# Kernel optimization log

Hardware: AMD Instinct MI355X
Metric: run time of the kernel (lower is better)

Reference implementation:

```python
import jax, jax.numpy as jnp
import numpy as np
import itertools, functools, operator

NUM_RBF = 32
CUTOFF = 5.0
METRIC = (1, 1, 1)


def _count_bits(x):
    return bin(x).count("1")


def _sign_euclidean(a, b):
    a >>= 1
    s = 0
    while a:
        s += _count_bits(a & b)
        a >>= 1
    return 1 if (s & 1) == 0 else -1


def build_cayley(metric):
    """Dense [2^n, 2^n, 2^n] geometric multiplication (Cayley) table, shortlex blade order."""
    n = len(metric)
    blade_sets = itertools.chain.from_iterable(
        itertools.combinations([1 << i for i in range(n)], r) for r in range(n + 1)
    )
    index_to_bitmap = [functools.reduce(operator.or_, t, 0) for t in blade_sets]
    bitmap_to_index = {b: i for i, b in enumerate(index_to_bitmap)}
    N = 2 ** n
    cayley = np.zeros((N, N, N), dtype=np.float32)
    for i in range(N):
        bi = index_to_bitmap[i]
        for j in range(N):
            bj = index_to_bitmap[j]
            sign = _sign_euclidean(bi, bj)
            bm = bi & bj
            k = 0
            while bm:
                if bm & 1:
                    sign *= metric[k]
                k += 1
                bm >>= 1
            cayley[i, bitmap_to_index[bi ^ bj], j] = sign
    return cayley


CAYLEY = jnp.asarray(build_cayley(METRIC))  # [8,8,8], sparse +/-1 structure


def geometric_product(a, b):
    # torch: einsum('...i,ijk,...k->...j', a, cayley, b)
    return jnp.einsum('...i,ijk,...k->...j', a, CAYLEY, b)


def setup_inputs() -> dict:
    key = jax.random.key(0)
    k0, k1, k2, k3, k4, k5 = jax.random.split(key, 6)
    N, E, C = 50000, 800000, 16
    h = jax.random.normal(k0, (N, C, 8), jnp.float32)
    pos = jax.random.uniform(k1, (N, 3), jnp.float32) * 10.0
    edge_index = jax.random.randint(k2, (2, E), 0, N, jnp.int32)
    W_rbf = jax.random.normal(k3, (NUM_RBF, C), jnp.float32) / np.sqrt(NUM_RBF)
    W_out = jax.random.normal(k4, (C, C), jnp.float32) / np.sqrt(C)
    W_sgp = jax.random.normal(k5, (C, C), jnp.float32) / np.sqrt(C)
    return {"h": h, "pos": pos, "edge_index": edge_index,
            "W_rbf": W_rbf, "W_out": W_out, "W_sgp": W_sgp}


def reference(h, pos, edge_index, W_rbf, W_out, W_sgp):
    N, C, B = h.shape
    src, dst = edge_index[0], edge_index[1]

    # relative geometry
    rel = pos[dst] - pos[src]                                  # [E,3]
    dist = jnp.sqrt(jnp.sum(rel * rel, axis=-1) + 1e-12)       # [E]

    # embed unit relative vector as a grade-1 multivector (blades 1..3)
    rel_mv = jnp.zeros((rel.shape[0], 1, B), h.dtype)
    rel_mv = rel_mv.at[:, 0, 1:4].set(rel / dist[:, None])     # [E,1,8]

    # radial weights: gaussian smearing -> linear -> cosine cutoff envelope
    mus = jnp.linspace(0.0, CUTOFF, NUM_RBF, dtype=h.dtype)
    gamma = (NUM_RBF / CUTOFF) ** 2
    rbf = jnp.exp(-gamma * (dist[:, None] - mus) ** 2)         # [E,32]
    env = 0.5 * (jnp.cos(jnp.pi * dist / CUTOFF) + 1.0) * (dist < CUTOFF)
    w_e = (rbf @ W_rbf) * env[:, None]                          # [E,C]

    # equivariant messages: geometric product against edge multivector
    msg = geometric_product(h[src], rel_mv) * w_e[..., None]   # [E,C,8]
    agg = jax.ops.segment_sum(msg, dst, num_segments=N)        # [N,C,8]

    # MVLinear channel mixing (shared across blades)
    out = jnp.einsum('nci,co->noi', agg, W_out)                # [N,C,8]

    # MACE-style higher-order: steerable geometric product self-interaction
    q = jnp.einsum('nci,co->noi', h, W_sgp)                    # [N,C,8]
    return out + geometric_product(out, q)
```

## Files before the change

kernel.cpp:

```cpp
#include <hip/hip_runtime.h>

#define CUTOFF 5.0f
#define GAMMA 40.96f
#define MU_STEP 0.16129032f
#define INV_MU 6.2f
#define PI_F 3.14159265358979f
#define MAXDEG 24


__global__ __launch_bounds__(256) void k_fill_geom(
    const float* __restrict__ pos, const int* __restrict__ ei,
    int* __restrict__ deg, int* __restrict__ rec,
    float4* __restrict__ edata, int E)
{
    int e = blockIdx.x * 256 + threadIdx.x;
    if (e >= E) return;
    int src = ei[e], dst = ei[E + e];
    float dx = pos[dst*3+0] - pos[src*3+0];
    float dy = pos[dst*3+1] - pos[src*3+1];
    float dz = pos[dst*3+2] - pos[src*3+2];
    float d = sqrtf(dx*dx + dy*dy + dz*dz + 1e-12f);
    if (d < CUTOFF) {
        int slot = atomicAdd(&deg[dst], 1);
        if (slot < MAXDEG) {
            const float s = (0.5f * (__cosf(PI_F * d * (1.0f/CUTOFF)) + 1.0f)) / d;
            rec[dst*MAXDEG + slot] = src;
            edata[(size_t)dst*MAXDEG + slot] = make_float4(dx*s, dy*s, dz*s, d);
        }
    }
}

__global__ __launch_bounds__(256) void k_gather_finalize(
    const float* __restrict__ h,
    const int* __restrict__ rec, const int* __restrict__ deg,
    const float4* __restrict__ edata,
    const float* __restrict__ Wrbf, const float* __restrict__ Wout,
    const float* __restrict__ Wsgp, float* __restrict__ out, int N)
{
    __shared__ float s_wr[512];
    __shared__ float s_Wout[256];
    __shared__ float s_Wsgp[256];
    __shared__ float s_agg[16*132];
    __shared__ float s_h[16*132];

    const int t  = threadIdx.x;
    const int nl = t >> 4;
    const int c  = t & 15;
    const int lane  = t & 63;
    const int gbase = lane & 48;
    const long long nodeBase = (long long)blockIdx.x * 16;
    const long long n = nodeBase + nl;

    s_wr[t]       = Wrbf[t];
    s_wr[t + 256] = Wrbf[t + 256];
    s_Wout[t] = Wout[t];
    s_Wsgp[t] = Wsgp[t];

    for (int idx = t; idx < 512; idx += 256) {
        int nn = idx >> 5;
        int r  = idx & 31;
        long long node = nodeBase + nn;
        float4 vh = make_float4(0,0,0,0);
        if (node < N) vh = *(const float4*)(h + node*128 + (long long)r*4);
        *(float4*)(&s_h[nn*132 + r*4]) = vh;
    }
    __syncthreads();

    float m0=0,m1=0,m2=0,m3=0,m4=0,m5=0,m6=0,m7=0;
    if (n < N) {
        const int start = (int)n * MAXDEG;
        const int dg    = min(deg[n], MAXDEG);
        const int dgE   = dg & ~1;

        for (int base = 0; base < dgE; base += 2) {
            const int2 ss  = *(const int2*)(rec + start + base);
            const float4 g0 = edata[start + base];
            const float4 g1 = edata[start + base + 1];

            const float4* hp0 = (const float4*)(h + (((long long)ss.x*16 + c) << 3));
            const float4* hp1 = (const float4*)(h + (((long long)ss.y*16 + c) << 3));
            const float4 A0 = hp0[0], B0 = hp0[1];
            const float4 A1 = hp1[0], B1 = hp1[1];

            const int kl0 = min(max(0, __float2int_rn(g0.w * INV_MU) - 2), 27);
            const int kl1 = min(max(0, __float2int_rn(g1.w * INV_MU) - 2), 27);

            const int   sel   = c >> 3;
            const float dsel  = sel ? g1.w : g0.w;
            const int   klsel = sel ? kl1 : kl0;
            const float xx = dsel - MU_STEP * (float)(klsel + (c & 7));
            const float ee = __expf(-GAMMA * xx * xx);

            float w0 = 0.0f, w1 = 0.0f;
            #pragma unroll
            for (int j = 0; j < 5; ++j) {
                const float e0 = __shfl(ee, gbase + j);
                const float e1 = __shfl(ee, gbase + 8 + j);
                w0 += e0 * s_wr[(kl0 + j)*16 + c];
                w1 += e1 * s_wr[(kl1 + j)*16 + c];
            }

            m0 += (A0.y*g0.x + A0.z*g0.y + A0.w*g0.z)*w0 + (A1.y*g1.x + A1.z*g1.y + A1.w*g1.z)*w1;
            m1 += (A0.x*g0.x + B0.x*g0.y + B0.y*g0.z)*w0 + (A1.x*g1.x + B1.x*g1.y + B1.y*g1.z)*w1;
            m2 += (A0.x*g0.y - B0.x*g0.x + B0.z*g0.z)*w0 + (A1.x*g1.y - B1.x*g1.x + B1.z*g1.z)*w1;
            m3 += (A0.x*g0.z - B0.y*g0.x - B0.z*g0.y)*w0 + (A1.x*g1.z - B1.y*g1.x - B1.z*g1.y)*w1;
            m4 += (A0.y*g0.y - A0.z*g0.x + B0.w*g0.z)*w0 + (A1.y*g1.y - A1.z*g1.x + B1.w*g1.z)*w1;
            m5 += (A0.y*g0.z - A0.w*g0.x - B0.w*g0.y)*w0 + (A1.y*g1.z - A1.w*g1.x - B1.w*g1.y)*w1;
            m6 += (A0.z*g0.z - A0.w*g0.y + B0.w*g0.x)*w0 + (A1.z*g1.z - A1.w*g1.y + B1.w*g1.x)*w1;
            m7 += (B0.z*g0.x - B0.y*g0.y + B0.x*g0.z)*w0 + (B1.z*g1.x - B1.y*g1.y + B1.x*g1.z)*w1;
        }

        if (dg & 1) {
            const int s0 = rec[start + dgE];
            const float4 g0 = edata[start + dgE];
            const float4* hp0 = (const float4*)(h + (((long long)s0*16 + c) << 3));
            const float4 A0 = hp0[0], B0 = hp0[1];

            const int kl0 = min(max(0, __float2int_rn(g0.w * INV_MU) - 2), 27);
            const float xx = g0.w - MU_STEP * (float)(kl0 + (c & 7));
            const float ee = __expf(-GAMMA * xx * xx);

            float w0 = 0.0f;
            #pragma unroll
            for (int j = 0; j < 5; ++j)
                w0 += __shfl(ee, gbase + j) * s_wr[(kl0 + j)*16 + c];

            m0 += (A0.y*g0.x + A0.z*g0.y + A0.w*g0.z)*w0;
            m1 += (A0.x*g0.x + B0.x*g0.y + B0.y*g0.z)*w0;
            m2 += (A0.x*g0.y - B0.x*g0.x + B0.z*g0.z)*w0;
            m3 += (A0.x*g0.z - B0.y*g0.x - B0.z*g0.y)*w0;
            m4 += (A0.y*g0.y - A0.z*g0.x + B0.w*g0.z)*w0;
            m5 += (A0.y*g0.z - A0.w*g0.x - B0.w*g0.y)*w0;
            m6 += (A0.z*g0.z - A0.w*g0.y + B0.w*g0.x)*w0;
            m7 += (B0.z*g0.x - B0.y*g0.y + B0.x*g0.z)*w0;
        }
    }

    __syncthreads();
    float* ag = &s_agg[nl*132 + c*8];
    *(float4*)(ag)     = make_float4(m0, m1, m2, m3);
    *(float4*)(ag + 4) = make_float4(m4, m5, m6, m7);
    __syncthreads();

    const int o = c;
    const float* A = &s_agg[nl*132];
    const float* H = &s_h[nl*132];

    float o0=0,o1=0,o2=0,o3=0,o4=0,o5=0,o6=0,o7=0;
    float q0=0,q1=0,q2=0,q3=0,q4=0,q5=0,q6=0,q7=0;
    #pragma unroll
    for (int cc = 0; cc < 16; ++cc) {
        const float wo = s_Wout[cc*16 + o];
        const float ws = s_Wsgp[cc*16 + o];
        const float* a  = A + cc*8;
        const float* hh = H + cc*8;
        o0 += a[0]*wo; o1 += a[1]*wo; o2 += a[2]*wo; o3 += a[3]*wo;
        o4 += a[4]*wo; o5 += a[5]*wo; o6 += a[6]*wo; o7 += a[7]*wo;
        q0 += hh[0]*ws; q1 += hh[1]*ws; q2 += hh[2]*ws; q3 += hh[3]*ws;
        q4 += hh[4]*ws; q5 += hh[5]*ws; q6 += hh[6]*ws; q7 += hh[7]*ws;
    }

    const float r0 = o0 + (o0*q0 + o1*q1 + o2*q2 + o3*q3 - o4*q4 - o5*q5 - o6*q6 - o7*q7);
    const float r1 = o1 + (o0*q1 + o1*q0 - o2*q4 - o3*q5 + o4*q2 + o5*q3 - o6*q7 - o7*q6);
    const float r2 = o2 + (o0*q2 + o1*q4 + o2*q0 - o3*q6 - o4*q1 + o5*q7 + o6*q3 + o7*q5);
    const float r3 = o3 + (o0*q3 + o1*q5 + o2*q6 + o3*q0 - o4*q7 - o5*q1 - o6*q2 - o7*q4);
    const float r4 = o4 + (o0*q4 + o1*q2 - o2*q1 + o3*q7 + o4*q0 - o5*q6 + o6*q5 + o7*q3);
    const float r5 = o5 + (o0*q5 + o1*q3 - o2*q7 - o3*q1 + o4*q6 + o5*q0 - o6*q4 - o7*q2);
    const float r6 = o6 + (o0*q6 + o1*q7 + o2*q3 - o3*q2 - o4*q5 + o5*q4 + o6*q0 + o7*q1);
    const float r7 = o7 + (o0*q7 + o1*q6 - o2*q5 + o3*q4 + o4*q3 - o5*q2 + o6*q1 + o7*q0);

    if (n < N) {
        float* op = out + (n*16 + o)*8;
        *(float4*)(op)     = make_float4(r0, r1, r2, r3);
        *(float4*)(op + 4) = make_float4(r4, r5, r6, r7);
    }
}

extern "C" void kernel_launch(void* const* d_in, const int* in_sizes, int n_in,
                              void* d_out, int out_size, void* d_ws, size_t ws_size,
                              hipStream_t stream) {
    const float* h    = (const float*)d_in[0];
    const float* pos  = (const float*)d_in[1];
    const int*   ei   = (const int*)d_in[2];
    const float* Wrbf = (const float*)d_in[3];
    const float* Wout = (const float*)d_in[4];
    const float* Wsgp = (const float*)d_in[5];
    float* out = (float*)d_out;

    const int N = in_sizes[0] / 128;
    const int E = in_sizes[2] / 2;

    float4* edata = (float4*)d_ws;
    int* deg = (int*)(edata + (size_t)N * MAXDEG);
    int* rec = deg + N;

    hipMemsetAsync(deg, 0, (size_t)N * sizeof(int), stream);

    const int eBlocks = (E + 255) / 256;
    k_fill_geom<<<eBlocks, 256, 0, stream>>>(pos, ei, deg, rec, edata, E);

    const int gBlocks = (N + 15) / 16;
    k_gather_finalize<<<gBlocks, 256, 0, stream>>>(
        h, rec, deg, edata, Wrbf, Wout, Wsgp, out, N);
}
```

Baseline: 138.1 us.

## Split fused gather/finalize kernel into separate edge-gather and finalize kernels

The fused gather+finalize kernel is split in two. The edge gather writes per-node aggregates into the output buffer, and a second kernel reloads them together with h to do the channel mixing and the self-interaction geometric product. The aim is to cut shared memory and register pressure in the gather kernel so it can run with higher occupancy. The cost is an extra kernel launch and an extra round trip of the aggregate through global memory.

```diff
diff --git a/kernel.cpp b/kernel.cpp
--- a/kernel.cpp
+++ b/kernel.cpp
@@ -30,40 +30,24 @@
     }
 }
 
-__global__ __launch_bounds__(256) void k_gather_finalize(
+__global__ __launch_bounds__(256) void k_edge_gather(
     const float* __restrict__ h,
     const int* __restrict__ rec, const int* __restrict__ deg,
     const float4* __restrict__ edata,
-    const float* __restrict__ Wrbf, const float* __restrict__ Wout,
-    const float* __restrict__ Wsgp, float* __restrict__ out, int N)
+    const float* __restrict__ Wrbf,
+    float* __restrict__ out, int N)
 {
     __shared__ float s_wr[512];
-    __shared__ float s_Wout[256];
-    __shared__ float s_Wsgp[256];
-    __shared__ float s_agg[16*132];
-    __shared__ float s_h[16*132];
 
     const int t  = threadIdx.x;
     const int nl = t >> 4;
     const int c  = t & 15;
     const int lane  = t & 63;
     const int gbase = lane & 48;
-    const long long nodeBase = (long long)blockIdx.x * 16;
-    const long long n = nodeBase + nl;
+    const long long n = (long long)blockIdx.x * 16 + nl;
 
     s_wr[t]       = Wrbf[t];
     s_wr[t + 256] = Wrbf[t + 256];
-    s_Wout[t] = Wout[t];
-    s_Wsgp[t] = Wsgp[t];
-
-    for (int idx = t; idx < 512; idx += 256) {
-        int nn = idx >> 5;
-        int r  = idx & 31;
-        long long node = nodeBase + nn;
-        float4 vh = make_float4(0,0,0,0);
-        if (node < N) vh = *(const float4*)(h + node*128 + (long long)r*4);
-        *(float4*)(&s_h[nn*132 + r*4]) = vh;
-    }
     __syncthreads();
 
     float m0=0,m1=0,m2=0,m3=0,m4=0,m5=0,m6=0,m7=0;
@@ -134,24 +118,57 @@
             m6 += (A0.z*g0.z - A0.w*g0.y + B0.w*g0.x)*w0;
             m7 += (B0.z*g0.x - B0.y*g0.y + B0.x*g0.z)*w0;
         }
-    }
-
+
+        float* op = out + n*128 + (long long)c*8;
+        *(float4*)(op)     = make_float4(m0, m1, m2, m3);
+        *(float4*)(op + 4) = make_float4(m4, m5, m6, m7);
+    }
+}
+
+__global__ __launch_bounds__(256) void k_finalize(
+    const float* __restrict__ h,
+    const float* __restrict__ Wout, const float* __restrict__ Wsgp,
+    float* __restrict__ out, int N)
+{
+    __shared__ float s_Wout[256];
+    __shared__ float s_Wsgp[256];
+    __shared__ float s_a[16*132];
+    __shared__ float s_h[16*132];
+
+    const int t  = threadIdx.x;
+    const int nl = t >> 4;
+    const int c  = t & 15;
+    const long long nodeBase = (long long)blockIdx.x * 16;
+    const long long n = nodeBase + nl;
+
+    s_Wout[t] = Wout[t];
+    s_Wsgp[t] = Wsgp[t];
+
+    for (int idx = t; idx < 1024; idx += 256) {
+        const int half = idx >> 9;
+        const int j    = idx & 511;
+        const int nn   = j >> 5;
+        const int r    = j & 31;
+        const long long node = nodeBase + nn;
+        float4 v = make_float4(0,0,0,0);
+        if (node < N) {
+            const float* src = half ? (h + node*128) : (out + node*128);
+            v = *(const float4*)(src + (long long)r*4);
+        }
+        float* dst = half ? &s_h[nn*132 + r*4] : &s_a[nn*132 + r*4];
+        *(float4*)(dst) = v;
+    }
     __syncthreads();
-    float* ag = &s_agg[nl*132 + c*8];
-    *(float4*)(ag)     = make_float4(m0, m1, m2, m3);
-    *(float4*)(ag + 4) = make_float4(m4, m5, m6, m7);
-    __syncthreads();
-
-    const int o = c;
-    const float* A = &s_agg[nl*132];
+
+    const float* A = &s_a[nl*132];
     const float* H = &s_h[nl*132];
 
     float o0=0,o1=0,o2=0,o3=0,o4=0,o5=0,o6=0,o7=0;
     float q0=0,q1=0,q2=0,q3=0,q4=0,q5=0,q6=0,q7=0;
     #pragma unroll
     for (int cc = 0; cc < 16; ++cc) {
-        const float wo = s_Wout[cc*16 + o];
-        const float ws = s_Wsgp[cc*16 + o];
+        const float wo = s_Wout[cc*16 + c];
+        const float ws = s_Wsgp[cc*16 + c];
         const float* a  = A + cc*8;
         const float* hh = H + cc*8;
         o0 += a[0]*wo; o1 += a[1]*wo; o2 += a[2]*wo; o3 += a[3]*wo;
@@ -170,7 +187,7 @@
     const float r7 = o7 + (o0*q7 + o1*q6 - o2*q5 + o3*q4 + o4*q3 - o5*q2 + o6*q1 + o7*q0);
 
     if (n < N) {
-        float* op = out + (n*16 + o)*8;
+        float* op = out + (n*16 + c)*8;
         *(float4*)(op)     = make_float4(r0, r1, r2, r3);
         *(float4*)(op + 4) = make_float4(r4, r5, r6, r7);
     }
@@ -200,6 +217,8 @@
     k_fill_geom<<<eBlocks, 256, 0, stream>>>(pos, ei, deg, rec, edata, E);
 
     const int gBlocks = (N + 15) / 16;
-    k_gather_finalize<<<gBlocks, 256, 0, stream>>>(
-        h, rec, deg, edata, Wrbf, Wout, Wsgp, out, N);
-}
+    k_edge_gather<<<gBlocks, 256, 0, stream>>>(
+        h, rec, deg, edata, Wrbf, out, N);
+    k_finalize<<<gBlocks, 256, 0, stream>>>(
+        h, Wout, Wsgp, out, N);
+}
```

After: 151.2 us. 1.1x slower.

## Split each node's edge gather across two half-warps and divide finalize work

Applied to the files above, without the earlier changes.

Each block now handles 8 nodes instead of 16, with two 16-thread groups per node that take alternating edge pairs. The two partial aggregates are reduced through shared memory. The finalize stage is also split: one half computes the W_sgp projection while the other sums the partials, and then the first half does the output mixing and geometric product. The goal is more parallelism on the latency-bound gather, since there are only about 16 edges per node. The cost is an extra shared-memory reduction, an extra barrier, and idle threads during the final stage.

```diff
diff --git a/kernel.cpp b/kernel.cpp
--- a/kernel.cpp
+++ b/kernel.cpp
@@ -40,15 +40,17 @@
     __shared__ float s_wr[512];
     __shared__ float s_Wout[256];
     __shared__ float s_Wsgp[256];
-    __shared__ float s_agg[16*132];
-    __shared__ float s_h[16*132];
-
-    const int t  = threadIdx.x;
-    const int nl = t >> 4;
-    const int c  = t & 15;
-    const int lane  = t & 63;
+    __shared__ float s_h[8*132];
+    __shared__ float s_agg[2*8*132];
+    __shared__ float s_q[8*132];
+
+    const int t    = threadIdx.x;
+    const int nl   = t >> 5;
+    const int half = (t >> 4) & 1;
+    const int c    = t & 15;
+    const int lane = t & 63;
     const int gbase = lane & 48;
-    const long long nodeBase = (long long)blockIdx.x * 16;
+    const long long nodeBase = (long long)blockIdx.x * 8;
     const long long n = nodeBase + nl;
 
     s_wr[t]       = Wrbf[t];
@@ -56,10 +58,10 @@
     s_Wout[t] = Wout[t];
     s_Wsgp[t] = Wsgp[t];
 
-    for (int idx = t; idx < 512; idx += 256) {
-        int nn = idx >> 5;
-        int r  = idx & 31;
-        long long node = nodeBase + nn;
+    {
+        const int nn = t >> 5;
+        const int r  = t & 31;
+        const long long node = nodeBase + nn;
         float4 vh = make_float4(0,0,0,0);
         if (node < N) vh = *(const float4*)(h + node*128 + (long long)r*4);
         *(float4*)(&s_h[nn*132 + r*4]) = vh;
@@ -70,9 +72,8 @@
     if (n < N) {
         const int start = (int)n * MAXDEG;
         const int dg    = min(deg[n], MAXDEG);
-        const int dgE   = dg & ~1;
-
-        for (int base = 0; base < dgE; base += 2) {
+
+        for (int base = half*2; base + 1 < dg; base += 4) {
             const int2 ss  = *(const int2*)(rec + start + base);
             const float4 g0 = edata[start + base];
             const float4 g1 = edata[start + base + 1];
@@ -110,7 +111,8 @@
             m7 += (B0.z*g0.x - B0.y*g0.y + B0.x*g0.z)*w0 + (B1.z*g1.x - B1.y*g1.y + B1.x*g1.z)*w1;
         }
 
-        if (dg & 1) {
+        if ((dg & 1) && (((dg >> 1) & 1) == half)) {
+            const int dgE = dg & ~1;
             const int s0 = rec[start + dgE];
             const float4 g0 = edata[start + dgE];
             const float4* hp0 = (const float4*)(h + (((long long)s0*16 + c) << 3));
@@ -136,41 +138,64 @@
         }
     }
 
-    __syncthreads();
-    float* ag = &s_agg[nl*132 + c*8];
+    float* ag = &s_agg[(half*8 + nl)*132 + c*8];
     *(float4*)(ag)     = make_float4(m0, m1, m2, m3);
     *(float4*)(ag + 4) = make_float4(m4, m5, m6, m7);
     __syncthreads();
 
-    const int o = c;
-    const float* A = &s_agg[nl*132];
-    const float* H = &s_h[nl*132];
-
-    float o0=0,o1=0,o2=0,o3=0,o4=0,o5=0,o6=0,o7=0;
-    float q0=0,q1=0,q2=0,q3=0,q4=0,q5=0,q6=0,q7=0;
-    #pragma unroll
-    for (int cc = 0; cc < 16; ++cc) {
-        const float wo = s_Wout[cc*16 + o];
-        const float ws = s_Wsgp[cc*16 + o];
-        const float* a  = A + cc*8;
-        const float* hh = H + cc*8;
-        o0 += a[0]*wo; o1 += a[1]*wo; o2 += a[2]*wo; o3 += a[3]*wo;
-        o4 += a[4]*wo; o5 += a[5]*wo; o6 += a[6]*wo; o7 += a[7]*wo;
-        q0 += hh[0]*ws; q1 += hh[1]*ws; q2 += hh[2]*ws; q3 += hh[3]*ws;
-        q4 += hh[4]*ws; q5 += hh[5]*ws; q6 += hh[6]*ws; q7 += hh[7]*ws;
-    }
-
-    const float r0 = o0 + (o0*q0 + o1*q1 + o2*q2 + o3*q3 - o4*q4 - o5*q5 - o6*q6 - o7*q7);
-    const float r1 = o1 + (o0*q1 + o1*q0 - o2*q4 - o3*q5 + o4*q2 + o5*q3 - o6*q7 - o7*q6);
-    const float r2 = o2 + (o0*q2 + o1*q4 + o2*q0 - o3*q6 - o4*q1 + o5*q7 + o6*q3 + o7*q5);
-    const float r3 = o3 + (o0*q3 + o1*q5 + o2*q6 + o3*q0 - o4*q7 - o5*q1 - o6*q2 - o7*q4);
-    const float r4 = o4 + (o0*q4 + o1*q2 - o2*q1 + o3*q7 + o4*q0 - o5*q6 + o6*q5 + o7*q3);
-    const float r5 = o5 + (o0*q5 + o1*q3 - o2*q7 - o3*q1 + o4*q6 + o5*q0 - o6*q4 - o7*q2);
-    const float r6 = o6 + (o0*q6 + o1*q7 + o2*q3 - o3*q2 - o4*q5 + o5*q4 + o6*q0 + o7*q1);
-    const float r7 = o7 + (o0*q7 + o1*q6 - o2*q5 + o3*q4 + o4*q3 - o5*q2 + o6*q1 + o7*q0);
-
-    if (n < N) {
-        float* op = out + (n*16 + o)*8;
+    const int idx0 = nl*16 + c;
+
+    if (half == 0) {
+        #pragma unroll
+        for (int f = idx0; f < 256; f += 128) {
+            const int node = f >> 5;
+            const int elem = (f & 31) << 2;
+            float4* d = (float4*)&s_agg[node*132 + elem];
+            const float4 s = *(const float4*)&s_agg[(8 + node)*132 + elem];
+            float4 v = *d;
+            v.x += s.x; v.y += s.y; v.z += s.z; v.w += s.w;
+            *d = v;
+        }
+    } else {
+        float q0=0,q1=0,q2=0,q3=0,q4=0,q5=0,q6=0,q7=0;
+        const float* H = &s_h[nl*132];
+        #pragma unroll
+        for (int cc = 0; cc < 16; ++cc) {
+            const float ws = s_Wsgp[cc*16 + c];
+            const float* hh = H + cc*8;
+            q0 += hh[0]*ws; q1 += hh[1]*ws; q2 += hh[2]*ws; q3 += hh[3]*ws;
+            q4 += hh[4]*ws; q5 += hh[5]*ws; q6 += hh[6]*ws; q7 += hh[7]*ws;
+        }
+        float* qp = &s_q[nl*132 + c*8];
+        *(float4*)(qp)     = make_float4(q0, q1, q2, q3);
+        *(float4*)(qp + 4) = make_float4(q4, q5, q6, q7);
+    }
+    __syncthreads();
+
+    if (half == 0 && n < N) {
+        float o0=0,o1=0,o2=0,o3=0,o4=0,o5=0,o6=0,o7=0;
+        const float* A = &s_agg[nl*132];
+        #pragma unroll
+        for (int cc = 0; cc < 16; ++cc) {
+            const float wo = s_Wout[cc*16 + c];
+            const float* a = A + cc*8;
+            o0 += a[0]*wo; o1 += a[1]*wo; o2 += a[2]*wo; o3 += a[3]*wo;
+            o4 += a[4]*wo; o5 += a[5]*wo; o6 += a[6]*wo; o7 += a[7]*wo;
+        }
+        const float* qq = &s_q[nl*132 + c*8];
+        const float q0 = qq[0], q1 = qq[1], q2 = qq[2], q3 = qq[3];
+        const float q4 = qq[4], q5 = qq[5], q6 = qq[6], q7 = qq[7];
+
+        const float r0 = o0 + (o0*q0 + o1*q1 + o2*q2 + o3*q3 - o4*q4 - o5*q5 - o6*q6 - o7*q7);
+        const float r1 = o1 + (o0*q1 + o1*q0 - o2*q4 - o3*q5 + o4*q2 + o5*q3 - o6*q7 - o7*q6);
+        const float r2 = o2 + (o0*q2 + o1*q4 + o2*q0 - o3*q6 - o4*q1 + o5*q7 + o6*q3 + o7*q5);
+        const float r3 = o3 + (o0*q3 + o1*q5 + o2*q6 + o3*q0 - o4*q7 - o5*q1 - o6*q2 - o7*q4);
+        const float r4 = o4 + (o0*q4 + o1*q2 - o2*q1 + o3*q7 + o4*q0 - o5*q6 + o6*q5 + o7*q3);
+        const float r5 = o5 + (o0*q5 + o1*q3 - o2*q7 - o3*q1 + o4*q6 + o5*q0 - o6*q4 - o7*q2);
+        const float r6 = o6 + (o0*q6 + o1*q7 + o2*q3 - o3*q2 - o4*q5 + o5*q4 + o6*q0 + o7*q1);
+        const float r7 = o7 + (o0*q7 + o1*q6 - o2*q5 + o3*q4 + o4*q3 - o5*q2 + o6*q1 + o7*q0);
+
+        float* op = out + (n*16 + c)*8;
         *(float4*)(op)     = make_float4(r0, r1, r2, r3);
         *(float4*)(op + 4) = make_float4(r4, r5, r6, r7);
     }
@@ -199,7 +224,7 @@
     const int eBlocks = (E + 255) / 256;
     k_fill_geom<<<eBlocks, 256, 0, stream>>>(pos, ei, deg, rec, edata, E);
 
-    const int gBlocks = (N + 15) / 16;
+    const int gBlocks = (N + 7) / 8;
     k_gather_finalize<<<gBlocks, 256, 0, stream>>>(
         h, rec, deg, edata, Wrbf, Wout, Wsgp, out, N);
 }
```

New measurement: 145.4 us. +5.3%, slower.
